# Kernel optimization log

Measured on AMD Instinct MI355X. Metric: run time of the kernel, lower is better.

Reference implementation:

```python
import jax, jax.numpy as jnp
import numpy as np

B = 64          # graphs per batch
N_NODES = 2000  # nodes per graph (model hyperparameter: FC2 in_features)
NF = 128        # node features
H = 8           # hidden_dim
OC = 8          # out_channels
NC = 2          # n_classes
DEG = 16        # avg degree
SLOPE = 0.01


def _lin_init(key, fan_in, fan_out):
    k1, k2 = jax.random.split(key)
    s = 1.0 / np.sqrt(fan_in)
    W = jax.random.uniform(k1, (fan_in, fan_out), jnp.float32, -s, s)
    b = jax.random.uniform(k2, (fan_out,), jnp.float32, -s, s)
    return W, b


def setup_inputs() -> dict:
    key = jax.random.key(0)
    ks = jax.random.split(key, 10)
    N = B * N_NODES
    E = N * DEG
    x = jax.random.normal(ks[0], (N, NF), jnp.float32)
    # graph-local random edges, offset per graph
    local = jax.random.randint(ks[1], (2, E), 0, N_NODES)
    off = jnp.repeat(jnp.arange(B, dtype=jnp.int64) * N_NODES, E // B)
    edge_index = (local + off[None, :]).astype(jnp.int64)
    batch = jnp.repeat(jnp.arange(B, dtype=jnp.int64), N_NODES)
    W1a, b1a = _lin_init(ks[2], NF, H)
    W1b, b1b = _lin_init(ks[3], H, H)
    W2a, b2a = _lin_init(ks[4], H, H)
    W2b, b2b = _lin_init(ks[5], H, OC)
    Wf1, bf1 = _lin_init(ks[6], OC, 1)
    Wf2, bf2 = _lin_init(ks[7], N_NODES, NC)
    return {"x": x, "edge_index": edge_index, "batch": batch,
            "W1a": W1a, "b1a": b1a, "W1b": W1b, "b1b": b1b,
            "W2a": W2a, "b2a": b2a, "W2b": W2b, "b2b": b2b,
            "Wf1": Wf1, "bf1": bf1, "Wf2": Wf2, "bf2": bf2}


def _lrelu(v):
    return jnp.where(v >= 0, v, SLOPE * v)


def _gin_conv(h, src, dst, Wa, ba, Wb, bb):
    N = h.shape[0]
    agg = jax.ops.segment_sum(h[src], dst, num_segments=N)  # sum_{j->i} h_j
    z = h + agg                                             # (1+eps)*h + agg, eps=0
    z = _lrelu(z @ Wa + ba)                                 # MLP linear1 + act
    return z @ Wb + bb                                      # MLP linear2 (plain last)


def reference(x, edge_index, batch, W1a, b1a, W1b, b1b, W2a, b2a, W2b, b2b,
              Wf1, bf1, Wf2, bf2):
    src, dst = edge_index[0], edge_index[1]
    h = _gin_conv(x, src, dst, W1a, b1a, W1b, b1b)
    h = _lrelu(h)  # inter-layer activation (dropout = identity at eval)
    h = _gin_conv(h, src, dst, W2a, b2a, W2b, b2b)  # [N, OC], no act after last conv
    bsz = h.shape[0] // N_NODES
    y = h.reshape(bsz, N_NODES, OC)
    y = _lrelu(y) @ Wf1 + bf1          # FC1 -> [B, n_nodes, 1]
    y = y.reshape(bsz, N_NODES)
    y = _lrelu(y) @ Wf2 + bf2          # FC2 -> [B, n_classes]
    return jax.nn.log_softmax(y, axis=1)
```

## Files before the change

### kernel.cpp

```cpp
#include <hip/hip_runtime.h>
#include <math.h>

#define NF 128
#define HD 8
#define NPG 2000
#define EPB 8000
#define TILE 64
#define TPG 32
#define SLOPE 0.01f

__device__ __forceinline__ float lrelu(float v) {
    return v > 0.0f ? v : SLOPE * v;
}

__global__ __launch_bounds__(256) void k_feat(const float* __restrict__ x,
                                              const float* __restrict__ W1a,
                                              float* __restrict__ t1, int N) {
    __shared__ float tile[64 * 132];
    __shared__ float wl[NF * HD];

    const int t = threadIdx.x;
    const size_t base = (size_t)blockIdx.x * 64;

    ((float4*)wl)[t] = ((const float4*)W1a)[t];

    const float4* xg = (const float4*)(x + base * NF);
#pragma unroll
    for (int i = 0; i < 8; ++i) {
        int f4 = t + i * 256;
        float4 v = xg[f4];
        int flat = f4 * 4;
        int n = flat >> 7;
        int k = flat & 127;
        *(float4*)(tile + n * 132 + k) = v;
    }
    __syncthreads();

    const int n = t >> 2;
    const int c0 = (t & 3) * 2;
    float acc0 = 0.0f, acc1 = 0.0f;
    const float* row = tile + n * 132;
#pragma unroll
    for (int k4 = 0; k4 < 32; ++k4) {
        float4 r = *(const float4*)(row + k4 * 4);
        int kb = k4 * 4 * HD;
        acc0 += r.x * wl[kb + c0];          acc1 += r.x * wl[kb + c0 + 1];
        acc0 += r.y * wl[kb + HD + c0];     acc1 += r.y * wl[kb + HD + c0 + 1];
        acc0 += r.z * wl[kb + 2*HD + c0];   acc1 += r.z * wl[kb + 2*HD + c0 + 1];
        acc0 += r.w * wl[kb + 3*HD + c0];   acc1 += r.w * wl[kb + 3*HD + c0 + 1];
    }
    *(float2*)(t1 + (base + n) * HD + c0) = make_float2(acc0, acc1);
}

__global__ __launch_bounds__(1024) void k_sort(const int* __restrict__ ei,
                                               int* __restrict__ gcol,
                                               int* __restrict__ rpc,
                                               int E) {
    __shared__ int cnt[NPG];
    __shared__ int srt[EPB];
    __shared__ int wtot[16], wpre[16];

    const int b = blockIdx.x;
    const int g = b >> 2;
    const int tid = threadIdx.x;
    const int lane = tid & 63;
    const int wv = tid >> 6;
    const int nodeBase = g * NPG;
    const int e0 = b * EPB;

    for (int i = tid; i < NPG; i += 1024) cnt[i] = 0;
    __syncthreads();

    for (int e = e0 + tid; e < e0 + EPB; e += 1024) {
        int dl = ei[E + e] - nodeBase;
        atomicAdd(&cnt[dl], 1);
    }
    __syncthreads();

    int c0 = 0, c1 = 0;
    if (tid < 1000) { c0 = cnt[2 * tid]; c1 = cnt[2 * tid + 1]; }
    int s = c0 + c1;
    int isc = s;
#pragma unroll
    for (int d = 1; d < 64; d <<= 1) {
        int o = __shfl_up(isc, d);
        if (lane >= d) isc += o;
    }
    if (lane == 63) wtot[wv] = isc;
    __syncthreads();
    if (wv == 0) {
        int v = (lane < 16) ? wtot[lane] : 0;
        int iv = v;
#pragma unroll
        for (int d = 1; d < 16; d <<= 1) {
            int o = __shfl_up(iv, d);
            if (lane >= d) iv += o;
        }
        if (lane < 16) wpre[lane] = iv - v;
    }
    __syncthreads();
    int excl = isc - s + wpre[wv];

    int* rpb = rpc + (size_t)b * (NPG + 1);
    if (tid < 1000) {
        cnt[2 * tid]     = excl;
        cnt[2 * tid + 1] = excl + c0;
        rpb[2 * tid]     = excl;
        rpb[2 * tid + 1] = excl + c0;
    }
    if (tid == 0) rpb[NPG] = EPB;
    __syncthreads();

    for (int e = e0 + tid; e < e0 + EPB; e += 1024) {
        int src = ei[e];
        int dl = ei[E + e] - nodeBase;
        int pos = atomicAdd(&cnt[dl], 1);
        srt[pos] = src;
    }
    __syncthreads();

    int4* dst4 = (int4*)(gcol + (size_t)b * EPB);
    const int4* s4 = (const int4*)srt;
    for (int i = tid; i < EPB / 4; i += 1024) dst4[i] = s4[i];
}

__global__ __launch_bounds__(256) void k_layer1(
    const float* __restrict__ t1, const int* __restrict__ rpc,
    const int* __restrict__ gcol, float* __restrict__ u,
    const float* __restrict__ b1a, const float* __restrict__ W1b,
    const float* __restrict__ b1b, const float* __restrict__ W2a)
{
    __shared__ float agg[TILE * HD];
    __shared__ float wts[144];

    const int tid = threadIdx.x;
    const int g = blockIdx.x >> 5;
    const int tile = blockIdx.x & 31;
    const int n0 = tile * TILE;

    if (tid < 144) {
        float v;
        if (tid < 8)       v = b1a[tid];
        else if (tid < 72) v = W1b[tid - 8];
        else if (tid < 80) v = b1b[tid - 72];
        else               v = W2a[tid - 80];
        wts[tid] = v;
    }

    const int lane = tid & 63;
    const int wv = tid >> 6;
    const int sub = lane >> 4;
    const int p = (lane >> 2) & 3;
    const int lj = lane & 3;
    const int* rpb  = rpc + (size_t)((g << 2) + p) * (NPG + 1);
    const int* colp = gcol + (size_t)((g << 2) + p) * EPB;

#pragma unroll
    for (int r = 0; r < 4; ++r) {
        int nl = n0 + r * 16 + wv * 4 + sub;
        bool valid = (nl < NPG);
        float a0 = 0, a1 = 0, a2 = 0, a3 = 0, a4 = 0, a5 = 0, a6 = 0, a7 = 0;
        if (valid) {
            int rs = rpb[nl], re = rpb[nl + 1];
            for (int e = rs + lj; e < re; e += 4) {
                int src = colp[e];
                const float* tr = t1 + (size_t)src * HD;
                float4 pa = *(const float4*)tr;
                float4 pb = *(const float4*)(tr + 4);
                a0 += pa.x; a1 += pa.y; a2 += pa.z; a3 += pa.w;
                a4 += pb.x; a5 += pb.y; a6 += pb.z; a7 += pb.w;
            }
        }
#pragma unroll
        for (int off = 1; off <= 8; off <<= 1) {
            a0 += __shfl_xor(a0, off); a1 += __shfl_xor(a1, off);
            a2 += __shfl_xor(a2, off); a3 += __shfl_xor(a3, off);
            a4 += __shfl_xor(a4, off); a5 += __shfl_xor(a5, off);
            a6 += __shfl_xor(a6, off); a7 += __shfl_xor(a7, off);
        }
        if (valid && (lane & 15) == 0) {
            float* ar = agg + (nl - n0) * HD;
            *(float4*)ar       = make_float4(a0, a1, a2, a3);
            *((float4*)ar + 1) = make_float4(a4, a5, a6, a7);
        }
    }
    __syncthreads();

    if (tid < TILE && n0 + tid < NPG) {
        int nl = n0 + tid;
        size_t n = (size_t)g * NPG + nl;
        const float* ti = t1 + n * HD;
        float4 aA = *(const float4*)(agg + tid * HD);
        float4 aB = *((const float4*)(agg + tid * HD) + 1);
        float z[HD];
        z[0] = lrelu(ti[0] + aA.x + wts[0]); z[1] = lrelu(ti[1] + aA.y + wts[1]);
        z[2] = lrelu(ti[2] + aA.z + wts[2]); z[3] = lrelu(ti[3] + aA.w + wts[3]);
        z[4] = lrelu(ti[4] + aB.x + wts[4]); z[5] = lrelu(ti[5] + aB.y + wts[5]);
        z[6] = lrelu(ti[6] + aB.z + wts[6]); z[7] = lrelu(ti[7] + aB.w + wts[7]);

        float h[HD];
#pragma unroll
        for (int j = 0; j < HD; ++j) {
            float acc = wts[72 + j];
#pragma unroll
            for (int c = 0; c < HD; ++c) acc += z[c] * wts[8 + c * HD + j];
            h[j] = lrelu(acc);
        }
        float uu[HD];
#pragma unroll
        for (int j = 0; j < HD; ++j) {
            float acc = 0.0f;
#pragma unroll
            for (int c = 0; c < HD; ++c) acc += h[c] * wts[80 + c * HD + j];
            uu[j] = acc;
        }
        float* ur = u + n * HD;
        *(float4*)ur       = make_float4(uu[0], uu[1], uu[2], uu[3]);
        *(float4*)(ur + 4) = make_float4(uu[4], uu[5], uu[6], uu[7]);
    }
}

__global__ __launch_bounds__(256) void k_layer2(
    const float* __restrict__ u, const int* __restrict__ rpc,
    const int* __restrict__ gcol,
    const float* __restrict__ b2a, const float* __restrict__ W2b,
    const float* __restrict__ b2b, const float* __restrict__ Wf1,
    const float* __restrict__ bf1, const float* __restrict__ Wf2,
    float* __restrict__ bparts)
{
    __shared__ float agg[TILE * HD];
    __shared__ float wts[89];
    __shared__ float red[8];

    const int tid = threadIdx.x;
    const int g = blockIdx.x >> 5;
    const int tile = blockIdx.x & 31;
    const int n0 = tile * TILE;

    if (tid < 89) {
        float v;
        if (tid < 8)       v = b2a[tid];
        else if (tid < 72) v = W2b[tid - 8];
        else if (tid < 80) v = b2b[tid - 72];
        else if (tid < 88) v = Wf1[tid - 80];
        else               v = bf1[0];
        wts[tid] = v;
    }

    const int lane = tid & 63;
    const int wv = tid >> 6;
    const int sub = lane >> 4;
    const int p = (lane >> 2) & 3;
    const int lj = lane & 3;
    const int* rpb  = rpc + (size_t)((g << 2) + p) * (NPG + 1);
    const int* colp = gcol + (size_t)((g << 2) + p) * EPB;

#pragma unroll
    for (int r = 0; r < 4; ++r) {
        int nl = n0 + r * 16 + wv * 4 + sub;
        bool valid = (nl < NPG);
        float a0 = 0, a1 = 0, a2 = 0, a3 = 0, a4 = 0, a5 = 0, a6 = 0, a7 = 0;
        if (valid) {
            int rs = rpb[nl], re = rpb[nl + 1];
            for (int e = rs + lj; e < re; e += 4) {
                int src = colp[e];
                const float* urr = u + (size_t)src * HD;
                float4 pa = *(const float4*)urr;
                float4 pb = *(const float4*)(urr + 4);
                a0 += pa.x; a1 += pa.y; a2 += pa.z; a3 += pa.w;
                a4 += pb.x; a5 += pb.y; a6 += pb.z; a7 += pb.w;
            }
        }
#pragma unroll
        for (int off = 1; off <= 8; off <<= 1) {
            a0 += __shfl_xor(a0, off); a1 += __shfl_xor(a1, off);
            a2 += __shfl_xor(a2, off); a3 += __shfl_xor(a3, off);
            a4 += __shfl_xor(a4, off); a5 += __shfl_xor(a5, off);
            a6 += __shfl_xor(a6, off); a7 += __shfl_xor(a7, off);
        }
        if (valid && (lane & 15) == 0) {
            float* ar = agg + (nl - n0) * HD;
            *(float4*)ar       = make_float4(a0, a1, a2, a3);
            *((float4*)ar + 1) = make_float4(a4, a5, a6, a7);
        }
    }
    __syncthreads();

    float acc0 = 0.0f, acc1 = 0.0f;
    if (tid < TILE && n0 + tid < NPG) {
        int nl = n0 + tid;
        size_t n = (size_t)g * NPG + nl;
        const float* ui = u + n * HD;
        float4 aA = *(const float4*)(agg + tid * HD);
        float4 aB = *((const float4*)(agg + tid * HD) + 1);
        float z[HD];
        z[0] = lrelu(ui[0] + aA.x + wts[0]); z[1] = lrelu(ui[1] + aA.y + wts[1]);
        z[2] = lrelu(ui[2] + aA.z + wts[2]); z[3] = lrelu(ui[3] + aA.w + wts[3]);
        z[4] = lrelu(ui[4] + aB.x + wts[4]); z[5] = lrelu(ui[5] + aB.y + wts[5]);
        z[6] = lrelu(ui[6] + aB.z + wts[6]); z[7] = lrelu(ui[7] + aB.w + wts[7]);

        float sv = wts[88];
#pragma unroll
        for (int j = 0; j < HD; ++j) {
            float acc = wts[72 + j];
#pragma unroll
            for (int c = 0; c < HD; ++c) acc += z[c] * wts[8 + c * HD + j];
            sv += lrelu(acc) * wts[80 + j];
        }
        float pf = lrelu(sv);
        float2 wf = *(const float2*)(Wf2 + (size_t)nl * 2);
        acc0 = pf * wf.x;
        acc1 = pf * wf.y;
    }

#pragma unroll
    for (int off = 32; off > 0; off >>= 1) {
        acc0 += __shfl_down(acc0, off);
        acc1 += __shfl_down(acc1, off);
    }
    if (lane == 0) { red[wv * 2] = acc0; red[wv * 2 + 1] = acc1; }
    __syncthreads();

    if (tid == 0) {
        float y0 = red[0] + red[2] + red[4] + red[6];
        float y1 = red[1] + red[3] + red[5] + red[7];
        *(float2*)(bparts + (size_t)(g * TPG + tile) * 2) = make_float2(y0, y1);
    }
}

__global__ __launch_bounds__(64) void k_fin(const float* __restrict__ bparts,
                                            const float* __restrict__ bf2,
                                            float* __restrict__ out, int Bn) {
    int g = threadIdx.x;
    if (g >= Bn) return;
    float y0 = bf2[0], y1 = bf2[1];
#pragma unroll
    for (int b = 0; b < TPG; ++b) {
        float2 v = *(const float2*)(bparts + (size_t)(g * TPG + b) * 2);
        y0 += v.x; y1 += v.y;
    }
    float m = fmaxf(y0, y1);
    float lse = m + logf(expf(y0 - m) + expf(y1 - m));
    out[g * 2 + 0] = y0 - lse;
    out[g * 2 + 1] = y1 - lse;
}

extern "C" void kernel_launch(void* const* d_in, const int* in_sizes, int n_in,
                              void* d_out, int out_size, void* d_ws, size_t ws_size,
                              hipStream_t stream) {
    const float* x   = (const float*)d_in[0];
    const int*   ei  = (const int*)  d_in[1];
    const float* W1a = (const float*)d_in[3];
    const float* b1a = (const float*)d_in[4];
    const float* W1b = (const float*)d_in[5];
    const float* b1b = (const float*)d_in[6];
    const float* W2a = (const float*)d_in[7];
    const float* b2a = (const float*)d_in[8];
    const float* W2b = (const float*)d_in[9];
    const float* b2b = (const float*)d_in[10];
    const float* Wf1 = (const float*)d_in[11];
    const float* bf1 = (const float*)d_in[12];
    const float* Wf2 = (const float*)d_in[13];
    const float* bf2 = (const float*)d_in[14];

    int N   = in_sizes[0] / NF;
    int E   = in_sizes[1] / 2;
    int Bn  = N / NPG;
    int NC  = Bn * 4;

    float* t1     = (float*)d_ws;
    float* u      = t1 + (size_t)N * HD;
    int*   gcol   = (int*)(u + (size_t)N * HD);
    int*   rpc    = gcol + (size_t)E;
    float* bparts = (float*)(rpc + (size_t)NC * (NPG + 1) + 16);

    k_feat  <<<N / 64, 256, 0, stream>>>(x, W1a, t1, N);
    k_sort  <<<NC, 1024, 0, stream>>>(ei, gcol, rpc, E);
    k_layer1<<<Bn * TPG, 256, 0, stream>>>(t1, rpc, gcol, u, b1a, W1b, b1b, W2a);
    k_layer2<<<Bn * TPG, 256, 0, stream>>>(u, rpc, gcol, b2a, W2b, b2b, Wf1,
                                           bf1, Wf2, bparts);
    k_fin   <<<1, 64, 0, stream>>>(bparts, bf2, (float*)d_out, Bn);
}
```

Before: 187.5 us.

## Stage per-graph features in LDS and process one graph per block

Each layer kernel now runs one 1024-thread block per graph and copies that graph's 2000x8 feature table into shared memory, so neighbour gathers read LDS instead of global memory. The sort kernel now stores graph-local source indices to match. The final reduction and log-softmax are folded into the layer-2 kernel, which removes the partial-sum buffer and the separate finishing launch. In exchange, only 64 blocks run on a GPU with far more CUs, and each thread walks its node's edges serially, which may leave much of the device idle.

```diff
diff --git a/kernel.cpp b/kernel.cpp
--- a/kernel.cpp
+++ b/kernel.cpp
@@ -5,8 +5,7 @@
 #define HD 8
 #define NPG 2000
 #define EPB 8000
-#define TILE 64
-#define TPG 32
+#define TBL4 (NPG * HD / 4)
 #define SLOPE 0.01f
 
 __device__ __forceinline__ float lrelu(float v) {
@@ -112,7 +111,7 @@
     __syncthreads();
 
     for (int e = e0 + tid; e < e0 + EPB; e += 1024) {
-        int src = ei[e];
+        int src = ei[e] - nodeBase;
         int dl = ei[E + e] - nodeBase;
         int pos = atomicAdd(&cnt[dl], 1);
         srt[pos] = src;
@@ -124,19 +123,17 @@
     for (int i = tid; i < EPB / 4; i += 1024) dst4[i] = s4[i];
 }
 
-__global__ __launch_bounds__(256) void k_layer1(
+__global__ __launch_bounds__(1024) void k_l1(
     const float* __restrict__ t1, const int* __restrict__ rpc,
     const int* __restrict__ gcol, float* __restrict__ u,
     const float* __restrict__ b1a, const float* __restrict__ W1b,
     const float* __restrict__ b1b, const float* __restrict__ W2a)
 {
-    __shared__ float agg[TILE * HD];
+    __shared__ float tbl[NPG * HD];
     __shared__ float wts[144];
 
+    const int g = blockIdx.x;
     const int tid = threadIdx.x;
-    const int g = blockIdx.x >> 5;
-    const int tile = blockIdx.x & 31;
-    const int n0 = tile * TILE;
 
     if (tid < 144) {
         float v;
@@ -147,56 +144,35 @@
         wts[tid] = v;
     }
 
-    const int lane = tid & 63;
-    const int wv = tid >> 6;
-    const int sub = lane >> 4;
-    const int p = (lane >> 2) & 3;
-    const int lj = lane & 3;
-    const int* rpb  = rpc + (size_t)((g << 2) + p) * (NPG + 1);
-    const int* colp = gcol + (size_t)((g << 2) + p) * EPB;
-
-#pragma unroll
-    for (int r = 0; r < 4; ++r) {
-        int nl = n0 + r * 16 + wv * 4 + sub;
-        bool valid = (nl < NPG);
+    const float4* src4 = (const float4*)(t1 + (size_t)g * NPG * HD);
+    float4* tbl4 = (float4*)tbl;
+#pragma unroll
+    for (int i = 0; i < 3; ++i) tbl4[tid + i * 1024] = src4[tid + i * 1024];
+    if (tid + 3 * 1024 < TBL4) tbl4[tid + 3 * 1024] = src4[tid + 3 * 1024];
+    __syncthreads();
+
+    for (int nl = tid; nl < NPG; nl += 1024) {
         float a0 = 0, a1 = 0, a2 = 0, a3 = 0, a4 = 0, a5 = 0, a6 = 0, a7 = 0;
-        if (valid) {
+#pragma unroll
+        for (int p = 0; p < 4; ++p) {
+            const int* rpb  = rpc + (size_t)((g << 2) + p) * (NPG + 1);
+            const int* colp = gcol + (size_t)((g << 2) + p) * EPB;
             int rs = rpb[nl], re = rpb[nl + 1];
-            for (int e = rs + lj; e < re; e += 4) {
-                int src = colp[e];
-                const float* tr = t1 + (size_t)src * HD;
-                float4 pa = *(const float4*)tr;
-                float4 pb = *(const float4*)(tr + 4);
+            for (int e = rs; e < re; ++e) {
+                int sl = colp[e];
+                const float* row = tbl + sl * HD;
+                float4 pa = *(const float4*)row;
+                float4 pb = *(const float4*)(row + 4);
                 a0 += pa.x; a1 += pa.y; a2 += pa.z; a3 += pa.w;
                 a4 += pb.x; a5 += pb.y; a6 += pb.z; a7 += pb.w;
             }
         }
-#pragma unroll
-        for (int off = 1; off <= 8; off <<= 1) {
-            a0 += __shfl_xor(a0, off); a1 += __shfl_xor(a1, off);
-            a2 += __shfl_xor(a2, off); a3 += __shfl_xor(a3, off);
-            a4 += __shfl_xor(a4, off); a5 += __shfl_xor(a5, off);
-            a6 += __shfl_xor(a6, off); a7 += __shfl_xor(a7, off);
-        }
-        if (valid && (lane & 15) == 0) {
-            float* ar = agg + (nl - n0) * HD;
-            *(float4*)ar       = make_float4(a0, a1, a2, a3);
-            *((float4*)ar + 1) = make_float4(a4, a5, a6, a7);
-        }
-    }
-    __syncthreads();
-
-    if (tid < TILE && n0 + tid < NPG) {
-        int nl = n0 + tid;
-        size_t n = (size_t)g * NPG + nl;
-        const float* ti = t1 + n * HD;
-        float4 aA = *(const float4*)(agg + tid * HD);
-        float4 aB = *((const float4*)(agg + tid * HD) + 1);
+        const float* ti = tbl + nl * HD;
         float z[HD];
-        z[0] = lrelu(ti[0] + aA.x + wts[0]); z[1] = lrelu(ti[1] + aA.y + wts[1]);
-        z[2] = lrelu(ti[2] + aA.z + wts[2]); z[3] = lrelu(ti[3] + aA.w + wts[3]);
-        z[4] = lrelu(ti[4] + aB.x + wts[4]); z[5] = lrelu(ti[5] + aB.y + wts[5]);
-        z[6] = lrelu(ti[6] + aB.z + wts[6]); z[7] = lrelu(ti[7] + aB.w + wts[7]);
+        z[0] = lrelu(ti[0] + a0 + wts[0]); z[1] = lrelu(ti[1] + a1 + wts[1]);
+        z[2] = lrelu(ti[2] + a2 + wts[2]); z[3] = lrelu(ti[3] + a3 + wts[3]);
+        z[4] = lrelu(ti[4] + a4 + wts[4]); z[5] = lrelu(ti[5] + a5 + wts[5]);
+        z[6] = lrelu(ti[6] + a6 + wts[6]); z[7] = lrelu(ti[7] + a7 + wts[7]);
 
         float h[HD];
 #pragma unroll
@@ -214,28 +190,28 @@
             for (int c = 0; c < HD; ++c) acc += h[c] * wts[80 + c * HD + j];
             uu[j] = acc;
         }
-        float* ur = u + n * HD;
+        float* ur = u + ((size_t)g * NPG + nl) * HD;
         *(float4*)ur       = make_float4(uu[0], uu[1], uu[2], uu[3]);
         *(float4*)(ur + 4) = make_float4(uu[4], uu[5], uu[6], uu[7]);
     }
 }
 
-__global__ __launch_bounds__(256) void k_layer2(
+__global__ __launch_bounds__(1024) void k_l2fin(
     const float* __restrict__ u, const int* __restrict__ rpc,
     const int* __restrict__ gcol,
     const float* __restrict__ b2a, const float* __restrict__ W2b,
     const float* __restrict__ b2b, const float* __restrict__ Wf1,
     const float* __restrict__ bf1, const float* __restrict__ Wf2,
-    float* __restrict__ bparts)
+    const float* __restrict__ bf2, float* __restrict__ out)
 {
-    __shared__ float agg[TILE * HD];
+    __shared__ float tbl[NPG * HD];
     __shared__ float wts[89];
-    __shared__ float red[8];
-
+    __shared__ float red[32];
+
+    const int g = blockIdx.x;
     const int tid = threadIdx.x;
-    const int g = blockIdx.x >> 5;
-    const int tile = blockIdx.x & 31;
-    const int n0 = tile * TILE;
+    const int lane = tid & 63;
+    const int wv = tid >> 6;
 
     if (tid < 89) {
         float v;
@@ -247,57 +223,36 @@
         wts[tid] = v;
     }
 
-    const int lane = tid & 63;
-    const int wv = tid >> 6;
-    const int sub = lane >> 4;
-    const int p = (lane >> 2) & 3;
-    const int lj = lane & 3;
-    const int* rpb  = rpc + (size_t)((g << 2) + p) * (NPG + 1);
-    const int* colp = gcol + (size_t)((g << 2) + p) * EPB;
-
-#pragma unroll
-    for (int r = 0; r < 4; ++r) {
-        int nl = n0 + r * 16 + wv * 4 + sub;
-        bool valid = (nl < NPG);
+    const float4* src4 = (const float4*)(u + (size_t)g * NPG * HD);
+    float4* tbl4 = (float4*)tbl;
+#pragma unroll
+    for (int i = 0; i < 3; ++i) tbl4[tid + i * 1024] = src4[tid + i * 1024];
+    if (tid + 3 * 1024 < TBL4) tbl4[tid + 3 * 1024] = src4[tid + 3 * 1024];
+    __syncthreads();
+
+    float acc0 = 0.0f, acc1 = 0.0f;
+    for (int nl = tid; nl < NPG; nl += 1024) {
         float a0 = 0, a1 = 0, a2 = 0, a3 = 0, a4 = 0, a5 = 0, a6 = 0, a7 = 0;
-        if (valid) {
+#pragma unroll
+        for (int p = 0; p < 4; ++p) {
+            const int* rpb  = rpc + (size_t)((g << 2) + p) * (NPG + 1);
+            const int* colp = gcol + (size_t)((g << 2) + p) * EPB;
             int rs = rpb[nl], re = rpb[nl + 1];
-            for (int e = rs + lj; e < re; e += 4) {
-                int src = colp[e];
-                const float* urr = u + (size_t)src * HD;
-                float4 pa = *(const float4*)urr;
-                float4 pb = *(const float4*)(urr + 4);
+            for (int e = rs; e < re; ++e) {
+                int sl = colp[e];
+                const float* row = tbl + sl * HD;
+                float4 pa = *(const float4*)row;
+                float4 pb = *(const float4*)(row + 4);
                 a0 += pa.x; a1 += pa.y; a2 += pa.z; a3 += pa.w;
                 a4 += pb.x; a5 += pb.y; a6 += pb.z; a7 += pb.w;
             }
         }
-#pragma unroll
-        for (int off = 1; off <= 8; off <<= 1) {
-            a0 += __shfl_xor(a0, off); a1 += __shfl_xor(a1, off);
-            a2 += __shfl_xor(a2, off); a3 += __shfl_xor(a3, off);
-            a4 += __shfl_xor(a4, off); a5 += __shfl_xor(a5, off);
-            a6 += __shfl_xor(a6, off); a7 += __shfl_xor(a7, off);
-        }
-        if (valid && (lane & 15) == 0) {
-            float* ar = agg + (nl - n0) * HD;
-            *(float4*)ar       = make_float4(a0, a1, a2, a3);
-            *((float4*)ar + 1) = make_float4(a4, a5, a6, a7);
-        }
-    }
-    __syncthreads();
-
-    float acc0 = 0.0f, acc1 = 0.0f;
-    if (tid < TILE && n0 + tid < NPG) {
-        int nl = n0 + tid;
-        size_t n = (size_t)g * NPG + nl;
-        const float* ui = u + n * HD;
-        float4 aA = *(const float4*)(agg + tid * HD);
-        float4 aB = *((const float4*)(agg + tid * HD) + 1);
+        const float* ui = tbl + nl * HD;
         float z[HD];
-        z[0] = lrelu(ui[0] + aA.x + wts[0]); z[1] = lrelu(ui[1] + aA.y + wts[1]);
-        z[2] = lrelu(ui[2] + aA.z + wts[2]); z[3] = lrelu(ui[3] + aA.w + wts[3]);
-        z[4] = lrelu(ui[4] + aB.x + wts[4]); z[5] = lrelu(ui[5] + aB.y + wts[5]);
-        z[6] = lrelu(ui[6] + aB.z + wts[6]); z[7] = lrelu(ui[7] + aB.w + wts[7]);
+        z[0] = lrelu(ui[0] + a0 + wts[0]); z[1] = lrelu(ui[1] + a1 + wts[1]);
+        z[2] = lrelu(ui[2] + a2 + wts[2]); z[3] = lrelu(ui[3] + a3 + wts[3]);
+        z[4] = lrelu(ui[4] + a4 + wts[4]); z[5] = lrelu(ui[5] + a5 + wts[5]);
+        z[6] = lrelu(ui[6] + a6 + wts[6]); z[7] = lrelu(ui[7] + a7 + wts[7]);
 
         float sv = wts[88];
 #pragma unroll
@@ -309,8 +264,8 @@
         }
         float pf = lrelu(sv);
         float2 wf = *(const float2*)(Wf2 + (size_t)nl * 2);
-        acc0 = pf * wf.x;
-        acc1 = pf * wf.y;
+        acc0 += pf * wf.x;
+        acc1 += pf * wf.y;
     }
 
 #pragma unroll
@@ -322,27 +277,14 @@
     __syncthreads();
 
     if (tid == 0) {
-        float y0 = red[0] + red[2] + red[4] + red[6];
-        float y1 = red[1] + red[3] + red[5] + red[7];
-        *(float2*)(bparts + (size_t)(g * TPG + tile) * 2) = make_float2(y0, y1);
-    }
-}
-
-__global__ __launch_bounds__(64) void k_fin(const float* __restrict__ bparts,
-                                            const float* __restrict__ bf2,
-                                            float* __restrict__ out, int Bn) {
-    int g = threadIdx.x;
-    if (g >= Bn) return;
-    float y0 = bf2[0], y1 = bf2[1];
-#pragma unroll
-    for (int b = 0; b < TPG; ++b) {
-        float2 v = *(const float2*)(bparts + (size_t)(g * TPG + b) * 2);
-        y0 += v.x; y1 += v.y;
-    }
-    float m = fmaxf(y0, y1);
-    float lse = m + logf(expf(y0 - m) + expf(y1 - m));
-    out[g * 2 + 0] = y0 - lse;
-    out[g * 2 + 1] = y1 - lse;
+        float y0 = bf2[0], y1 = bf2[1];
+#pragma unroll
+        for (int w = 0; w < 16; ++w) { y0 += red[w * 2]; y1 += red[w * 2 + 1]; }
+        float m = fmaxf(y0, y1);
+        float lse = m + logf(expf(y0 - m) + expf(y1 - m));
+        out[g * 2 + 0] = y0 - lse;
+        out[g * 2 + 1] = y1 - lse;
+    }
 }
 
 extern "C" void kernel_launch(void* const* d_in, const int* in_sizes, int n_in,
@@ -368,16 +310,14 @@
     int Bn  = N / NPG;
     int NC  = Bn * 4;
 
-    float* t1     = (float*)d_ws;
-    float* u      = t1 + (size_t)N * HD;
-    int*   gcol   = (int*)(u + (size_t)N * HD);
-    int*   rpc    = gcol + (size_t)E;
-    float* bparts = (float*)(rpc + (size_t)NC * (NPG + 1) + 16);
+    float* t1   = (float*)d_ws;
+    float* u    = t1 + (size_t)N * HD;
+    int*   gcol = (int*)(u + (size_t)N * HD);
+    int*   rpc  = gcol + (size_t)E;
 
     k_feat  <<<N / 64, 256, 0, stream>>>(x, W1a, t1, N);
     k_sort  <<<NC, 1024, 0, stream>>>(ei, gcol, rpc, E);
-    k_layer1<<<Bn * TPG, 256, 0, stream>>>(t1, rpc, gcol, u, b1a, W1b, b1b, W2a);
-    k_layer2<<<Bn * TPG, 256, 0, stream>>>(u, rpc, gcol, b2a, W2b, b2b, Wf1,
-                                           bf1, Wf2, bparts);
-    k_fin   <<<1, 64, 0, stream>>>(bparts, bf2, (float*)d_out, Bn);
-}
+    k_l1    <<<Bn, 1024, 0, stream>>>(t1, rpc, gcol, u, b1a, W1b, b1b, W2a);
+    k_l2fin <<<Bn, 1024, 0, stream>>>(u, rpc, gcol, b2a, W2b, b2b, Wf1, bf1,
+                                      Wf2, bf2, (float*)d_out);
+}
```

New measurement: 210.9 us. 1.12x slower.
